# Optimization experiments

Hardware: AMD Instinct MI355X
Metric: run time of the kernel (lower is better)

## Reference

```python
import jax, jax.numpy as jnp
import numpy as np

DIM = 384
FRACTION = 16   # quant_bits=16 -> fixed-point fraction bits
INTEGER = 16
WEIGHT_BITS = 5
SHIFT_MIN = -(2 ** (WEIGHT_BITS - 1) - 2)  # -14 (DeepShift shift_range for 5-bit)


def _ste(x, qx):
    # straight-through estimator: forward qx, backward identity
    return x + jax.lax.stop_gradient(qx - x)


def _clampabs(w, mn, mx):
    # clamp |w| into [mn, mx], preserving sign (zeros stay zero)
    return jnp.sign(w) * jnp.clip(jnp.abs(w), mn, mx)


def _round_power_of_2(w):
    # w -> sign(w) * 2^round(log2(|w|))
    shift = jnp.round(jnp.log2(jnp.maximum(jnp.abs(w), 1e-30)))
    return jnp.sign(w) * jnp.exp2(shift)


def _round_to_fixed(x, fraction=FRACTION, integer=INTEGER):
    delta = 2.0 ** (-fraction)
    bound = 2.0 ** (integer - 1)
    return jnp.clip(jnp.floor(x / delta) * delta, -bound, bound - 1)


def setup_inputs() -> dict:
    key = jax.random.key(0)
    k1, k2, k3 = jax.random.split(key, 3)
    x = jax.random.normal(k1, (32, DIM, 56, 56), dtype=jnp.float32)
    weight = jax.random.normal(k2, (DIM, 1, 3, 3), dtype=jnp.float32) * 0.1
    bias = jax.random.normal(k3, (DIM,), dtype=jnp.float32) * 0.01
    return {"x": x, "weight": weight, "bias": bias}


def reference(x, weight, bias):
    # weight: clamp magnitude to [2^-14, 2^0], then round to signed power of two (5-bit shift)
    w = _ste(weight, _clampabs(weight, 2.0 ** SHIFT_MIN, 1.0))
    w = _ste(w, _round_power_of_2(w))
    # activations / bias: 16-bit fixed-point rounding
    xq = _ste(x, _round_to_fixed(x))
    bq = _ste(bias, _round_to_fixed(bias))
    # depthwise 3x3 conv, stride 1, padding 1, groups = DIM
    out = jax.lax.conv_general_dilated(
        xq, w,
        window_strides=(1, 1),
        padding=((1, 1), (1, 1)),
        feature_group_count=DIM,
        dimension_numbers=("NCHW", "OIHW", "NCHW"),
    )
    return out + bq[None, :, None, None]
```

## Files before the change

### kernel.cpp

```cpp
#include <hip/hip_runtime.h>


#define DW_C     384
#define DW_H     56
#define DW_W     56
#define DW_HW    3136
#define SEG_ROWS 28
#define NW4      14

__device__ __forceinline__ float qfix(float v) {
    v = floorf(v * 65536.0f) * (1.0f / 65536.0f);
    return fminf(fmaxf(v, -32768.0f), 32767.0f);
}

struct Row { float l, a, b, c, d, r; };

__global__ __launch_bounds__(256) void quant_wb(
    const float* __restrict__ wgt, const float* __restrict__ bias,
    float* __restrict__ wq, float* __restrict__ bq)
{
    int i = blockIdx.x * 256 + threadIdx.x;
    if (i < DW_C * 9) {
        float wv = wgt[i];
        float aw = fabsf(wv);
        float cw = fminf(fmaxf(aw, 6.103515625e-05f ), 1.0f);
        float q  = exp2f(rintf(log2f(cw)));
        wq[i] = (wv > 0.0f) ? q : ((wv < 0.0f) ? -q : 0.0f);
    }
    if (i < DW_C) bq[i] = qfix(bias[i]);
}

template<bool PRE>
__global__ __launch_bounds__(256, 6) void peg_shift_stream(
    const float* __restrict__ x, const float* __restrict__ wgt,
    const float* __restrict__ bias, float* __restrict__ out,
    const float* __restrict__ wsq, const float* __restrict__ wsb)
{
    const int task = blockIdx.x * 256 + threadIdx.x;
    const int plane = task / 28;
    const int t28   = task - plane * 28;
    const int seg   = t28 / NW4;
    const int w4    = t28 - seg * NW4;
    const int c     = plane % DW_C;
    const int r0    = seg * SEG_ROWS;

    const bool hl = (w4 > 0);
    const bool hr = (w4 < NW4 - 1);

    float ww[9];
    float bqv;
    if (PRE) {
        const float* wp = wsq + c * 9;
#pragma unroll
        for (int t = 0; t < 9; ++t) ww[t] = wp[t];
        bqv = wsb[c];
    } else {
        const float* wp = wgt + c * 9;
#pragma unroll
        for (int t = 0; t < 9; ++t) {
            float wv = wp[t];
            float aw = fabsf(wv);
            float cw = fminf(fmaxf(aw, 6.103515625e-05f), 1.0f);
            float q  = exp2f(rintf(log2f(cw)));
            ww[t] = (wv > 0.0f) ? q : ((wv < 0.0f) ? -q : 0.0f);
        }
        bqv = qfix(bias[c]);
    }

    const float* xb = x + (size_t)plane * DW_HW + w4 * 4;

    auto loadq = [&](int rr) -> Row {
        Row q;
        if (rr >= 0 && rr < DW_H) {
            const float* p = xb + rr * DW_W;
            float4 m = *(const float4*)p;
            float lv = hl ? p[-1] : 0.0f;
            float rv = hr ? p[4]  : 0.0f;
            q.l = qfix(lv); q.a = qfix(m.x); q.b = qfix(m.y);
            q.c = qfix(m.z); q.d = qfix(m.w); q.r = qfix(rv);
        } else {
            q.l = q.a = q.b = q.c = q.d = q.r = 0.0f;
        }
        return q;
    };

    Row A = loadq(r0 - 1);
    Row B = loadq(r0);
    Row C = loadq(r0 + 1);

    float* ob = out + (size_t)plane * DW_HW + r0 * DW_W + w4 * 4;

#pragma unroll 4
    for (int i = 0; i < SEG_ROWS; ++i) {
        const int rr = r0 + i + 2;
        float4 pm; pm.x = pm.y = pm.z = pm.w = 0.0f;
        float pl = 0.0f, pr = 0.0f;
        if (rr < DW_H) {
            const float* p = xb + rr * DW_W;
            pm = *(const float4*)p;
            if (hl) pl = p[-1];
            if (hr) pr = p[4];
        }

        float o0 = bqv, o1 = bqv, o2 = bqv, o3 = bqv;
        o0 = fmaf(A.l, ww[0], fmaf(A.a, ww[1], fmaf(A.b, ww[2], o0)));
        o1 = fmaf(A.a, ww[0], fmaf(A.b, ww[1], fmaf(A.c, ww[2], o1)));
        o2 = fmaf(A.b, ww[0], fmaf(A.c, ww[1], fmaf(A.d, ww[2], o2)));
        o3 = fmaf(A.c, ww[0], fmaf(A.d, ww[1], fmaf(A.r, ww[2], o3)));
        o0 = fmaf(B.l, ww[3], fmaf(B.a, ww[4], fmaf(B.b, ww[5], o0)));
        o1 = fmaf(B.a, ww[3], fmaf(B.b, ww[4], fmaf(B.c, ww[5], o1)));
        o2 = fmaf(B.b, ww[3], fmaf(B.c, ww[4], fmaf(B.d, ww[5], o2)));
        o3 = fmaf(B.c, ww[3], fmaf(B.d, ww[4], fmaf(B.r, ww[5], o3)));
        o0 = fmaf(C.l, ww[6], fmaf(C.a, ww[7], fmaf(C.b, ww[8], o0)));
        o1 = fmaf(C.a, ww[6], fmaf(C.b, ww[7], fmaf(C.c, ww[8], o1)));
        o2 = fmaf(C.b, ww[6], fmaf(C.c, ww[7], fmaf(C.d, ww[8], o2)));
        o3 = fmaf(C.c, ww[6], fmaf(C.d, ww[7], fmaf(C.r, ww[8], o3)));

        float4 ov; ov.x = o0; ov.y = o1; ov.z = o2; ov.w = o3;
        *(float4*)ob = ov;
        ob += DW_W;

        A = B; B = C;
        C.l = qfix(pl);   C.a = qfix(pm.x); C.b = qfix(pm.y);
        C.c = qfix(pm.z); C.d = qfix(pm.w); C.r = qfix(pr);
    }
}

extern "C" void kernel_launch(void* const* d_in, const int* in_sizes, int n_in,
                              void* d_out, int out_size, void* d_ws, size_t ws_size,
                              hipStream_t stream) {
    const float* x = (const float*)d_in[0];
    const float* w = (const float*)d_in[1];
    const float* b = (const float*)d_in[2];
    float* out = (float*)d_out;

    int planes  = in_sizes[0] / DW_HW;
    int tasks   = planes * 28;
    int nblocks = (tasks + 255) / 256;

    size_t need = (size_t)(DW_C * 9 + DW_C) * sizeof(float);
    if (d_ws && ws_size >= need) {
        float* wq = (float*)d_ws;
        float* bq = wq + DW_C * 9;
        quant_wb<<<(DW_C * 9 + 255) / 256, 256, 0, stream>>>(w, b, wq, bq);
        peg_shift_stream<true><<<nblocks, 256, 0, stream>>>(x, w, b, out, wq, bq);
    } else {
        peg_shift_stream<false><<<nblocks, 256, 0, stream>>>(x, w, b, out, nullptr, nullptr);
    }
}
```

Baseline: 307.6 us.

## Split planes into three row segments, prefetch two rows ahead, nontemporal stores

Each plane is now split into three row segments of 19/19/18 rows instead of two of 28, which raises the thread count, and the minimum-blocks hint goes from 6 to 8. Raw input rows are loaded two iterations ahead of use so load latency overlaps the FMAs, with quantisation deferred until the row is needed. Output is written with nontemporal stores to avoid cache pollution. The extra segment adds more halo-row re-reads, and the deeper prefetch raises register pressure under the tighter occupancy bound.

```diff
diff --git a/kernel.cpp b/kernel.cpp
--- a/kernel.cpp
+++ b/kernel.cpp
@@ -1,12 +1,13 @@
 #include <hip/hip_runtime.h>
 
 
-#define DW_C     384
-#define DW_H     56
-#define DW_W     56
-#define DW_HW    3136
-#define SEG_ROWS 28
-#define NW4      14
+#define DW_C   384
+#define DW_H   56
+#define DW_W   56
+#define DW_HW  3136
+#define NW4    14
+
+typedef float v4f __attribute__((ext_vector_type(4)));
 
 __device__ __forceinline__ float qfix(float v) {
     v = floorf(v * 65536.0f) * (1.0f / 65536.0f);
@@ -31,18 +32,23 @@
 }
 
 template<bool PRE>
-__global__ __launch_bounds__(256, 6) void peg_shift_stream(
+__global__ __launch_bounds__(256, 8) void peg_shift_stream(
     const float* __restrict__ x, const float* __restrict__ wgt,
     const float* __restrict__ bias, float* __restrict__ out,
-    const float* __restrict__ wsq, const float* __restrict__ wsb)
+    const float* __restrict__ wsq, const float* __restrict__ wsb,
+    int ntask)
 {
     const int task = blockIdx.x * 256 + threadIdx.x;
-    const int plane = task / 28;
-    const int t28   = task - plane * 28;
-    const int seg   = t28 / NW4;
-    const int w4    = t28 - seg * NW4;
+    if (task >= ntask) return;
+
+    const int plane = task / 42;
+    const int t42   = task - plane * 42;
+    const int seg   = t42 / NW4;
+    const int w4    = t42 - seg * NW4;
     const int c     = plane % DW_C;
-    const int r0    = seg * SEG_ROWS;
+    const int r0    = seg * 19;
+    const int n     = (seg == 2) ? 18 : 19;
+    const int rlim  = min(r0 + n + 1, DW_H);
 
     const bool hl = (w4 > 0);
     const bool hr = (w4 < NW4 - 1);
@@ -69,38 +75,36 @@
 
     const float* xb = x + (size_t)plane * DW_HW + w4 * 4;
 
-    auto loadq = [&](int rr) -> Row {
+    auto loadraw = [&](int rr, float4& m, float& lv, float& rv) {
+        m.x = m.y = m.z = m.w = 0.0f; lv = 0.0f; rv = 0.0f;
+        if (rr >= 0 && rr < rlim) {
+            const float* p = xb + rr * DW_W;
+            m = *(const float4*)p;
+            if (hl) lv = p[-1];
+            if (hr) rv = p[4];
+        }
+    };
+    auto quant = [&](const float4& m, float lv, float rv) -> Row {
         Row q;
-        if (rr >= 0 && rr < DW_H) {
-            const float* p = xb + rr * DW_W;
-            float4 m = *(const float4*)p;
-            float lv = hl ? p[-1] : 0.0f;
-            float rv = hr ? p[4]  : 0.0f;
-            q.l = qfix(lv); q.a = qfix(m.x); q.b = qfix(m.y);
-            q.c = qfix(m.z); q.d = qfix(m.w); q.r = qfix(rv);
-        } else {
-            q.l = q.a = q.b = q.c = q.d = q.r = 0.0f;
-        }
+        q.l = qfix(lv);  q.a = qfix(m.x); q.b = qfix(m.y);
+        q.c = qfix(m.z); q.d = qfix(m.w); q.r = qfix(rv);
         return q;
     };
 
-    Row A = loadq(r0 - 1);
-    Row B = loadq(r0);
-    Row C = loadq(r0 + 1);
+    float4 m0, m1, m2, mP, mQ;
+    float  l0, r0v, l1, r1v, l2, r2v, lP, rP, lQ, rQ;
+    loadraw(r0 - 1, m0, l0, r0v);
+    loadraw(r0,     m1, l1, r1v);
+    loadraw(r0 + 1, m2, l2, r2v);
+    loadraw(r0 + 2, mP, lP, rP);
+    Row A = quant(m0, l0, r0v);
+    Row B = quant(m1, l1, r1v);
+    Row C = quant(m2, l2, r2v);
 
     float* ob = out + (size_t)plane * DW_HW + r0 * DW_W + w4 * 4;
 
-#pragma unroll 4
-    for (int i = 0; i < SEG_ROWS; ++i) {
-        const int rr = r0 + i + 2;
-        float4 pm; pm.x = pm.y = pm.z = pm.w = 0.0f;
-        float pl = 0.0f, pr = 0.0f;
-        if (rr < DW_H) {
-            const float* p = xb + rr * DW_W;
-            pm = *(const float4*)p;
-            if (hl) pl = p[-1];
-            if (hr) pr = p[4];
-        }
+    for (int i = 0; i < n; ++i) {
+        loadraw(r0 + i + 3, mQ, lQ, rQ);
 
         float o0 = bqv, o1 = bqv, o2 = bqv, o3 = bqv;
         o0 = fmaf(A.l, ww[0], fmaf(A.a, ww[1], fmaf(A.b, ww[2], o0)));
@@ -116,13 +120,13 @@
         o2 = fmaf(C.b, ww[6], fmaf(C.c, ww[7], fmaf(C.d, ww[8], o2)));
         o3 = fmaf(C.c, ww[6], fmaf(C.d, ww[7], fmaf(C.r, ww[8], o3)));
 
-        float4 ov; ov.x = o0; ov.y = o1; ov.z = o2; ov.w = o3;
-        *(float4*)ob = ov;
+        v4f ov; ov.x = o0; ov.y = o1; ov.z = o2; ov.w = o3;
+        __builtin_nontemporal_store(ov, (v4f*)ob);
         ob += DW_W;
 
         A = B; B = C;
-        C.l = qfix(pl);   C.a = qfix(pm.x); C.b = qfix(pm.y);
-        C.c = qfix(pm.z); C.d = qfix(pm.w); C.r = qfix(pr);
+        C = quant(mP, lP, rP);
+        mP = mQ; lP = lQ; rP = rQ;
     }
 }
 
@@ -135,7 +139,7 @@
     float* out = (float*)d_out;
 
     int planes  = in_sizes[0] / DW_HW;
-    int tasks   = planes * 28;
+    int tasks   = planes * 42;
     int nblocks = (tasks + 255) / 256;
 
     size_t need = (size_t)(DW_C * 9 + DW_C) * sizeof(float);
@@ -143,8 +147,8 @@
         float* wq = (float*)d_ws;
         float* bq = wq + DW_C * 9;
         quant_wb<<<(DW_C * 9 + 255) / 256, 256, 0, stream>>>(w, b, wq, bq);
-        peg_shift_stream<true><<<nblocks, 256, 0, stream>>>(x, w, b, out, wq, bq);
+        peg_shift_stream<true><<<nblocks, 256, 0, stream>>>(x, w, b, out, wq, bq, tasks);
     } else {
-        peg_shift_stream<false><<<nblocks, 256, 0, stream>>>(x, w, b, out, nullptr, nullptr);
+        peg_shift_stream<false><<<nblocks, 256, 0, stream>>>(x, w, b, out, nullptr, nullptr, tasks);
     }
 }
```

After: 461.5 us. +50.0%, slower.

## Stage quantized input tiles in double-buffered LDS with register prefetch

Applied to the files above, without the earlier changes.

Replaces the per-thread row-streaming stencil with blocks that each process six planes in half-plane chunks staged through a double-buffered shared memory tile. The next chunk's global loads are issued into registers before computing the current chunk, then quantized and committed to the other buffer. The goal is to overlap global memory latency with compute and get coalesced float4 loads without scalar halo reads. In exchange it adds block-wide barriers per chunk, LDS traffic, and a 30/28 halo overfetch per half plane.

```diff
diff --git a/kernel.cpp b/kernel.cpp
--- a/kernel.cpp
+++ b/kernel.cpp
@@ -1,19 +1,27 @@
 #include <hip/hip_runtime.h>
 
 
-#define DW_C     384
-#define DW_H     56
-#define DW_W     56
-#define DW_HW    3136
-#define SEG_ROWS 28
-#define NW4      14
+#define DW_C    384
+#define DW_H    56
+#define DW_W    56
+#define DW_HW   3136
+#define NW4     14
+#define PPB     6
+#define CHUNKS  (PPB * 2)
+#define SROWS   30
+#define SFLOATS (SROWS * DW_W)
+#define SIDX_N  (SROWS * NW4)
+#define OIDX_N  (28 * NW4)
 
 __device__ __forceinline__ float qfix(float v) {
     v = floorf(v * 65536.0f) * (1.0f / 65536.0f);
     return fminf(fmaxf(v, -32768.0f), 32767.0f);
 }
 
-struct Row { float l, a, b, c, d, r; };
+__device__ __forceinline__ float4 qfix4(float4 v) {
+    v.x = qfix(v.x); v.y = qfix(v.y); v.z = qfix(v.z); v.w = qfix(v.w);
+    return v;
+}
 
 __global__ __launch_bounds__(256) void quant_wb(
     const float* __restrict__ wgt, const float* __restrict__ bias,
@@ -31,98 +39,111 @@
 }
 
 template<bool PRE>
-__global__ __launch_bounds__(256, 6) void peg_shift_stream(
+__global__ __launch_bounds__(256, 8) void peg_shift_pipe(
     const float* __restrict__ x, const float* __restrict__ wgt,
     const float* __restrict__ bias, float* __restrict__ out,
     const float* __restrict__ wsq, const float* __restrict__ wsb)
 {
-    const int task = blockIdx.x * 256 + threadIdx.x;
-    const int plane = task / 28;
-    const int t28   = task - plane * 28;
-    const int seg   = t28 / NW4;
-    const int w4    = t28 - seg * NW4;
-    const int c     = plane % DW_C;
-    const int r0    = seg * SEG_ROWS;
+    __shared__ float s[2][SFLOATS];
 
-    const bool hl = (w4 > 0);
-    const bool hr = (w4 < NW4 - 1);
+    const int tid = threadIdx.x;
+    const int p0  = blockIdx.x * PPB;
 
-    float ww[9];
-    float bqv;
-    if (PRE) {
-        const float* wp = wsq + c * 9;
-#pragma unroll
-        for (int t = 0; t < 9; ++t) ww[t] = wp[t];
-        bqv = wsb[c];
-    } else {
-        const float* wp = wgt + c * 9;
-#pragma unroll
-        for (int t = 0; t < 9; ++t) {
-            float wv = wp[t];
-            float aw = fabsf(wv);
-            float cw = fminf(fmaxf(aw, 6.103515625e-05f), 1.0f);
-            float q  = exp2f(rintf(log2f(cw)));
-            ww[t] = (wv > 0.0f) ? q : ((wv < 0.0f) ? -q : 0.0f);
+    const int  s0r = tid / NW4, s0c = tid - s0r * NW4;
+    const int  s1i = tid + 256;
+    const bool st1 = (s1i < SIDX_N);
+    const int  s1r = s1i / NW4, s1c = s1i - s1r * NW4;
+    const int  o1i = tid + 256;
+    const bool cp1 = (o1i < OIDX_N);
+    const int  o1r = o1i / NW4, o1c = o1i - o1r * NW4;
+
+    const int sw0 = s0r * DW_W + s0c * 4;
+    const int sw1 = s1r * DW_W + s1c * 4;
+
+    auto fetch = [&](int chunk, float4& a, float4& b) {
+        const int plane = p0 + (chunk >> 1);
+        const int half  = chunk & 1;
+        const float* xp = x + (size_t)plane * DW_HW;
+        const int g0 = half * 28 - 1 + s0r;
+        a.x = a.y = a.z = a.w = 0.0f;
+        if (g0 >= 0 && g0 < DW_H) a = *(const float4*)(xp + g0 * DW_W + s0c * 4);
+        b.x = b.y = b.z = b.w = 0.0f;
+        if (st1) {
+            const int g1 = half * 28 - 1 + s1r;
+            if (g1 >= 0 && g1 < DW_H) b = *(const float4*)(xp + g1 * DW_W + s1c * 4);
         }
-        bqv = qfix(bias[c]);
-    }
-
-    const float* xb = x + (size_t)plane * DW_HW + w4 * 4;
-
-    auto loadq = [&](int rr) -> Row {
-        Row q;
-        if (rr >= 0 && rr < DW_H) {
-            const float* p = xb + rr * DW_W;
-            float4 m = *(const float4*)p;
-            float lv = hl ? p[-1] : 0.0f;
-            float rv = hr ? p[4]  : 0.0f;
-            q.l = qfix(lv); q.a = qfix(m.x); q.b = qfix(m.y);
-            q.c = qfix(m.z); q.d = qfix(m.w); q.r = qfix(rv);
-        } else {
-            q.l = q.a = q.b = q.c = q.d = q.r = 0.0f;
-        }
-        return q;
+    };
+    auto commit = [&](float* buf, const float4& a, const float4& b) {
+        *(float4*)(buf + sw0) = qfix4(a);
+        if (st1) *(float4*)(buf + sw1) = qfix4(b);
     };
 
-    Row A = loadq(r0 - 1);
-    Row B = loadq(r0);
-    Row C = loadq(r0 + 1);
+    {
+        float4 a, b;
+        fetch(0, a, b);
+        commit(s[0], a, b);
+    }
+    __syncthreads();
 
-    float* ob = out + (size_t)plane * DW_HW + r0 * DW_W + w4 * 4;
+    for (int ch = 0; ch < CHUNKS; ++ch) {
+        const int plane = p0 + (ch >> 1);
+        const int half  = ch & 1;
+        const bool more = (ch + 1 < CHUNKS);
 
-#pragma unroll 4
-    for (int i = 0; i < SEG_ROWS; ++i) {
-        const int rr = r0 + i + 2;
-        float4 pm; pm.x = pm.y = pm.z = pm.w = 0.0f;
-        float pl = 0.0f, pr = 0.0f;
-        if (rr < DW_H) {
-            const float* p = xb + rr * DW_W;
-            pm = *(const float4*)p;
-            if (hl) pl = p[-1];
-            if (hr) pr = p[4];
+        float4 na, nb;
+        if (more) fetch(ch + 1, na, nb);
+
+        const int c = plane % DW_C;
+        float ww[9], bqv;
+        if (PRE) {
+            const float* wp = wsq + c * 9;
+#pragma unroll
+            for (int t = 0; t < 9; ++t) ww[t] = wp[t];
+            bqv = wsb[c];
+        } else {
+            const float* wp = wgt + c * 9;
+#pragma unroll
+            for (int t = 0; t < 9; ++t) {
+                float wv = wp[t];
+                float aw = fabsf(wv);
+                float cw = fminf(fmaxf(aw, 6.103515625e-05f), 1.0f);
+                float q  = exp2f(rintf(log2f(cw)));
+                ww[t] = (wv > 0.0f) ? q : ((wv < 0.0f) ? -q : 0.0f);
+            }
+            bqv = qfix(bias[c]);
         }
 
-        float o0 = bqv, o1 = bqv, o2 = bqv, o3 = bqv;
-        o0 = fmaf(A.l, ww[0], fmaf(A.a, ww[1], fmaf(A.b, ww[2], o0)));
-        o1 = fmaf(A.a, ww[0], fmaf(A.b, ww[1], fmaf(A.c, ww[2], o1)));
-        o2 = fmaf(A.b, ww[0], fmaf(A.c, ww[1], fmaf(A.d, ww[2], o2)));
-        o3 = fmaf(A.c, ww[0], fmaf(A.d, ww[1], fmaf(A.r, ww[2], o3)));
-        o0 = fmaf(B.l, ww[3], fmaf(B.a, ww[4], fmaf(B.b, ww[5], o0)));
-        o1 = fmaf(B.a, ww[3], fmaf(B.b, ww[4], fmaf(B.c, ww[5], o1)));
-        o2 = fmaf(B.b, ww[3], fmaf(B.c, ww[4], fmaf(B.d, ww[5], o2)));
-        o3 = fmaf(B.c, ww[3], fmaf(B.d, ww[4], fmaf(B.r, ww[5], o3)));
-        o0 = fmaf(C.l, ww[6], fmaf(C.a, ww[7], fmaf(C.b, ww[8], o0)));
-        o1 = fmaf(C.a, ww[6], fmaf(C.b, ww[7], fmaf(C.c, ww[8], o1)));
-        o2 = fmaf(C.b, ww[6], fmaf(C.c, ww[7], fmaf(C.d, ww[8], o2)));
-        o3 = fmaf(C.c, ww[6], fmaf(C.d, ww[7], fmaf(C.r, ww[8], o3)));
+        const float* buf = s[ch & 1];
+        float* op = out + (size_t)plane * DW_HW + half * 28 * DW_W;
 
-        float4 ov; ov.x = o0; ov.y = o1; ov.z = o2; ov.w = o3;
-        *(float4*)ob = ov;
-        ob += DW_W;
+#define ROWFMA(RP, HL, HR, W0, W1, W2) {                               \
+            const float* rp_ = (RP);                                   \
+            float4 m_ = *(const float4*)rp_;                           \
+            float L_ = (HL) ? rp_[-1] : 0.0f;                          \
+            float R_ = (HR) ? rp_[4]  : 0.0f;                          \
+            a0 = fmaf(L_,   W0, fmaf(m_.x, W1, fmaf(m_.y, W2, a0)));  \
+            a1 = fmaf(m_.x, W0, fmaf(m_.y, W1, fmaf(m_.z, W2, a1)));  \
+            a2 = fmaf(m_.y, W0, fmaf(m_.z, W1, fmaf(m_.w, W2, a2)));  \
+            a3 = fmaf(m_.z, W0, fmaf(m_.w, W1, fmaf(R_,   W2, a3))); }
 
-        A = B; B = C;
-        C.l = qfix(pl);   C.a = qfix(pm.x); C.b = qfix(pm.y);
-        C.c = qfix(pm.z); C.d = qfix(pm.w); C.r = qfix(pr);
+#define CGROUP(OR, OC, EN) if (EN) {                                   \
+            float a0 = bqv, a1 = bqv, a2 = bqv, a3 = bqv;              \
+            const bool hl_ = ((OC) > 0), hr_ = ((OC) < NW4 - 1);       \
+            const float* base = buf + (OR) * DW_W + (OC) * 4;          \
+            ROWFMA(base,            hl_, hr_, ww[0], ww[1], ww[2]);    \
+            ROWFMA(base + DW_W,     hl_, hr_, ww[3], ww[4], ww[5]);    \
+            ROWFMA(base + 2 * DW_W, hl_, hr_, ww[6], ww[7], ww[8]);    \
+            float4 ov_; ov_.x = a0; ov_.y = a1; ov_.z = a2; ov_.w = a3;\
+            *(float4*)(op + (OR) * DW_W + (OC) * 4) = ov_; }
+
+        CGROUP(s0r, s0c, true)
+        CGROUP(o1r, o1c, cp1)
+
+#undef CGROUP
+#undef ROWFMA
+
+        if (more) commit((float*)s[(ch + 1) & 1], na, nb);
+        __syncthreads();
     }
 }
 
@@ -135,16 +156,15 @@
     float* out = (float*)d_out;
 
     int planes  = in_sizes[0] / DW_HW;
-    int tasks   = planes * 28;
-    int nblocks = (tasks + 255) / 256;
+    int nblocks = planes / PPB;
 
     size_t need = (size_t)(DW_C * 9 + DW_C) * sizeof(float);
     if (d_ws && ws_size >= need) {
         float* wq = (float*)d_ws;
         float* bq = wq + DW_C * 9;
         quant_wb<<<(DW_C * 9 + 255) / 256, 256, 0, stream>>>(w, b, wq, bq);
-        peg_shift_stream<true><<<nblocks, 256, 0, stream>>>(x, w, b, out, wq, bq);
+        peg_shift_pipe<true><<<nblocks, 256, 0, stream>>>(x, w, b, out, wq, bq);
     } else {
-        peg_shift_stream<false><<<nblocks, 256, 0, stream>>>(x, w, b, out, nullptr, nullptr);
+        peg_shift_pipe<false><<<nblocks, 256, 0, stream>>>(x, w, b, out, nullptr, nullptr);
     }
 }
```

New measurement: 281.6 us. 8.5% less time.
